# Kernel tuning notes

Measured on AMD Instinct MI355X. Metric: run time of the kernel, lower is better.

The kernel has to match this reference:

```python
import jax, jax.numpy as jnp
import numpy as np

D = 1024
H = 4
HD = D // H
B = 256
L = 64
DILATIONS = (1, 4, 8, 16)


def setup_inputs() -> dict:
    key = jax.random.key(0)
    ks = jax.random.split(key, 12)
    s = 1.0 / np.sqrt(D)
    return {
        "x": jax.random.normal(ks[0], (B, D), jnp.float32),
        "hist": jax.random.normal(ks[1], (L, B, D), jnp.float32),
        "Wq": jax.random.normal(ks[2], (D, D), jnp.float32) * s,
        "bq": jnp.zeros((D,), jnp.float32),
        "Wk": jax.random.normal(ks[3], (D, D), jnp.float32) * s,
        "bk": jnp.zeros((D,), jnp.float32),
        "Wv": jax.random.normal(ks[4], (D, D), jnp.float32) * s,
        "bv": jnp.zeros((D,), jnp.float32),
        "Wo": jax.random.normal(ks[5], (D, D), jnp.float32) * s,
        "bo": jnp.zeros((D,), jnp.float32),
        "dil_w": jnp.full((len(DILATIONS),), 1.0 / len(DILATIONS), jnp.float32),
        "gamma": jnp.ones((D,), jnp.float32),
        "beta": jnp.zeros((D,), jnp.float32),
    }


def reference(x, hist, Wq, bq, Wk, bk, Wv, bv, Wo, bo, dil_w, gamma, beta):
    scale = 1.0 / np.sqrt(HD)
    q = (x @ Wq + bq).reshape(B, H, HD)  # (B, H, HD)
    attended = []
    for d in DILATIONS:
        # history frames at stride d, concatenated along dim 0 (faithful to torch.cat)
        frames = hist[::d].reshape(-1, D)              # (T', D), T' = ceil(L/d)*B
        k = (frames @ Wk + bk).reshape(-1, H, HD)      # (T', H, HD)
        v = (frames @ Wv + bv).reshape(-1, H, HD)
        s = jnp.einsum('bhd,thd->bht', q, k) * scale   # (B, H, T')
        a = jax.nn.softmax(s, axis=-1)
        attended.append(jnp.einsum('bht,thd->bhd', a, v).reshape(B, D))
    w = jax.nn.softmax(dil_w, axis=0)
    combined = sum(w[i] * attended[i] for i in range(len(DILATIONS)))
    y = x + combined @ Wo + bo
    mu = jnp.mean(y, axis=-1, keepdims=True)
    var = jnp.var(y, axis=-1, keepdims=True)
    return (y - mu) / jnp.sqrt(var + 1e-5) * gamma + beta
```

## Files before the change

kernel.cpp:

```cpp
#include <hip/hip_runtime.h>


#define DD    1024
#define TALL  16384

typedef _Float16 half8  __attribute__((ext_vector_type(8)));
typedef _Float16 half4v __attribute__((ext_vector_type(4)));
typedef float    floatx4 __attribute__((ext_vector_type(4)));
typedef unsigned int u32;

static const size_t OFF_WQT = 0;
static const size_t OFF_WKT = 2097152;
static const size_t OFF_WVT = 4194304;
static const size_t OFF_WOT = 6291456;
static const size_t OFF_XB  = 8388608;
static const size_t OFF_QS  = 8912896;
static const size_t OFF_HB  = 16777216;
static const size_t OFF_S   = OFF_HB;
static const size_t OFF_KB  = 50331648;
static const size_t OFF_VT  = 83886080;
static const size_t OFF_PART= 117440512;
static const size_t OFF_MT  = 134217728;
static const size_t OFF_CT  = 134221824;
static const size_t OFF_CB  = 134483968;
static const size_t OFF_CP  = 135008256;

__device__ __forceinline__ void gl_lds16(const void* g, void* l) {
  __builtin_amdgcn_global_load_lds((const __attribute__((address_space(1))) u32*)g,
                                   (__attribute__((address_space(3))) u32*)l, 16, 0, 0);
}

__global__ void wtrans_kernel(const float* __restrict__ W0, const float* __restrict__ W1,
                              const float* __restrict__ W2, const float* __restrict__ W3,
                              _Float16* __restrict__ T0, _Float16* __restrict__ T1,
                              _Float16* __restrict__ T2, _Float16* __restrict__ T3) {
  const float* W; _Float16* T;
  switch (blockIdx.z) {
    case 0: W = W0; T = T0; break;
    case 1: W = W1; T = T1; break;
    case 2: W = W2; T = T2; break;
    default: W = W3; T = T3; break;
  }
  __shared__ float tile[32][33];
  int tx = threadIdx.x & 31, ty = threadIdx.x >> 5;
  int k0 = blockIdx.x * 32, n0 = blockIdx.y * 32;
#pragma unroll
  for (int i = 0; i < 4; i++) {
    int r = ty + i * 8;
    tile[r][tx] = W[(size_t)(k0 + r) * DD + n0 + tx];
  }
  __syncthreads();
#pragma unroll
  for (int i = 0; i < 4; i++) {
    int r = ty + i * 8;
    T[(size_t)(n0 + r) * DD + k0 + tx] = (_Float16)tile[tx][r];
  }
}

__global__ void cvt_kernel(const float* __restrict__ in, _Float16* __restrict__ out, int n4) {
  int i = blockIdx.x * 256 + threadIdx.x;
  if (i >= n4) return;
  float4 v = ((const float4*)in)[i];
  half4v h = {(_Float16)v.x, (_Float16)v.y, (_Float16)v.z, (_Float16)v.w};
  *(half4v*)(out + 4 * (size_t)i) = h;
}

__device__ __forceinline__ void gemm_core(const _Float16* __restrict__ A, size_t lda,
                                          const _Float16* __restrict__ B, size_t ldb,
                                          int kIters, _Float16* As, _Float16* Bs,
                                          int tid, floatx4 acc[4][4]) {
  int lane = tid & 63, w = tid >> 6;
  int l15 = lane & 15, quad = lane >> 4;
  int wm = (w >> 1) * 64, wn = (w & 1) * 64;
  const char* gA0 = (const char*)(A + (size_t)(tid >> 2) * lda + (tid & 3) * 8);
  const char* gA1 = (const char*)(A + ((size_t)(tid >> 2) + 64) * lda + (tid & 3) * 8);
  const char* gB0 = (const char*)(B + (size_t)(tid >> 2) * ldb + (tid & 3) * 8);
  const char* gB1 = (const char*)(B + ((size_t)(tid >> 2) + 64) * ldb + (tid & 3) * 8);
  _Float16* lA0 = As + w * 512; _Float16* lA1 = As + 2048 + w * 512;
  _Float16* lB0 = Bs + w * 512; _Float16* lB1 = Bs + 2048 + w * 512;
  for (int kk = 0; kk < kIters; kk++) {
    __syncthreads();
    size_t off = (size_t)kk * 64;
    gl_lds16(gA0 + off, lA0);
    gl_lds16(gA1 + off, lA1);
    gl_lds16(gB0 + off, lB0);
    gl_lds16(gB1 + off, lB1);
    __syncthreads();
    half8 a[4];
#pragma unroll
    for (int mi = 0; mi < 4; mi++) a[mi] = *(const half8*)&As[(wm + mi * 16 + l15) * 32 + quad * 8];
#pragma unroll
    for (int ni = 0; ni < 4; ni++) {
      half8 b8 = *(const half8*)&Bs[(wn + ni * 16 + l15) * 32 + quad * 8];
#pragma unroll
      for (int mi = 0; mi < 4; mi++)
        acc[mi][ni] = __builtin_amdgcn_mfma_f32_16x16x32_f16(a[mi], b8, acc[mi][ni], 0, 0, 0);
    }
  }
}

template <bool OUTF32>
__launch_bounds__(256, 2)
__global__ void gemm_f16_kernel(const _Float16* __restrict__ A, size_t lda, size_t aoffz,
                                const _Float16* __restrict__ B, size_t ldb, size_t boffz,
                                int kIters, const float* __restrict__ bias, float scale,
                                void* __restrict__ C, size_t ldc, size_t coffz) {
  __shared__ __align__(16) _Float16 As[4096];
  __shared__ __align__(16) _Float16 Bs[4096];
  int tid = threadIdx.x;
  const _Float16* Ab = A + aoffz * blockIdx.z + (size_t)(blockIdx.y * 128) * lda;
  const _Float16* Bb = B + boffz * blockIdx.z + (size_t)(blockIdx.x * 128) * ldb;
  floatx4 acc[4][4];
  floatx4 zero = {0.f, 0.f, 0.f, 0.f};
#pragma unroll
  for (int a = 0; a < 4; a++)
#pragma unroll
    for (int b = 0; b < 4; b++) acc[a][b] = zero;
  gemm_core(Ab, lda, Bb, ldb, kIters, As, Bs, tid, acc);
  int lane = tid & 63, w = tid >> 6;
  int l15 = lane & 15, quad = lane >> 4;
  int wm = (w >> 1) * 64, wn = (w & 1) * 64;
#pragma unroll
  for (int mi = 0; mi < 4; mi++)
#pragma unroll
    for (int ni = 0; ni < 4; ni++) {
      int colg = blockIdx.x * 128 + wn + ni * 16 + l15;
      float bv = bias ? bias[colg] : 0.f;
#pragma unroll
      for (int r = 0; r < 4; r++) {
        int rowg = blockIdx.y * 128 + wm + mi * 16 + quad * 4 + r;
        float v = (acc[mi][ni][r] + bv) * scale;
        size_t idx = coffz * blockIdx.z + (size_t)rowg * ldc + colg;
        if (OUTF32) ((float*)C)[idx] = v;
        else ((_Float16*)C)[idx] = (_Float16)v;
      }
    }
}

__launch_bounds__(256, 2)
__global__ void gemm_kv_kernel(const _Float16* __restrict__ A,
                               const _Float16* __restrict__ WkT, const _Float16* __restrict__ WvT,
                               const float* __restrict__ bk, const float* __restrict__ bv,
                               _Float16* __restrict__ K, _Float16* __restrict__ Vt) {
  __shared__ __align__(16) _Float16 As[4096];
  __shared__ __align__(16) _Float16 Bk[4096];
  __shared__ __align__(16) _Float16 Bv[4096];
  int tid = threadIdx.x;
  int lane = tid & 63, w = tid >> 6;
  int l15 = lane & 15, quad = lane >> 4;
  int wm = (w >> 1) * 64, wn = (w & 1) * 64;
  int m0 = blockIdx.y * 128, n0 = blockIdx.x * 128;
  floatx4 accK[4][4], accV[4][4];
  floatx4 zero = {0.f, 0.f, 0.f, 0.f};
#pragma unroll
  for (int a = 0; a < 4; a++)
#pragma unroll
    for (int b = 0; b < 4; b++) { accK[a][b] = zero; accV[a][b] = zero; }
  const char* gA0 = (const char*)(A + ((size_t)m0 + (tid >> 2)) * 1024 + (tid & 3) * 8);
  const char* gA1 = gA0 + 64 * 1024 * 2;
  const char* gK0 = (const char*)(WkT + ((size_t)n0 + (tid >> 2)) * 1024 + (tid & 3) * 8);
  const char* gK1 = gK0 + 64 * 1024 * 2;
  const char* gV0 = (const char*)(WvT + ((size_t)n0 + (tid >> 2)) * 1024 + (tid & 3) * 8);
  const char* gV1 = gV0 + 64 * 1024 * 2;
  _Float16* lA0 = As + w * 512; _Float16* lA1 = As + 2048 + w * 512;
  _Float16* lK0 = Bk + w * 512; _Float16* lK1 = Bk + 2048 + w * 512;
  _Float16* lV0 = Bv + w * 512; _Float16* lV1 = Bv + 2048 + w * 512;
  for (int kk = 0; kk < 32; kk++) {
    __syncthreads();
    size_t off = (size_t)kk * 64;
    gl_lds16(gA0 + off, lA0); gl_lds16(gA1 + off, lA1);
    gl_lds16(gK0 + off, lK0); gl_lds16(gK1 + off, lK1);
    gl_lds16(gV0 + off, lV0); gl_lds16(gV1 + off, lV1);
    __syncthreads();
    half8 a[4];
#pragma unroll
    for (int mi = 0; mi < 4; mi++) a[mi] = *(const half8*)&As[(wm + mi * 16 + l15) * 32 + quad * 8];
#pragma unroll
    for (int ni = 0; ni < 4; ni++) {
      half8 k8 = *(const half8*)&Bk[(wn + ni * 16 + l15) * 32 + quad * 8];
      half8 v8 = *(const half8*)&Bv[(wn + ni * 16 + l15) * 32 + quad * 8];
#pragma unroll
      for (int mi = 0; mi < 4; mi++) {
        accK[mi][ni] = __builtin_amdgcn_mfma_f32_16x16x32_f16(a[mi], k8, accK[mi][ni], 0, 0, 0);
        accV[mi][ni] = __builtin_amdgcn_mfma_f32_16x16x32_f16(a[mi], v8, accV[mi][ni], 0, 0, 0);
      }
    }
  }
#pragma unroll
  for (int mi = 0; mi < 4; mi++)
#pragma unroll
    for (int ni = 0; ni < 4; ni++) {
      int col = n0 + wn + ni * 16 + l15;
      float bkv = bk[col], bvv = bv[col];
#pragma unroll
      for (int r = 0; r < 4; r++) {
        int row = m0 + wm + mi * 16 + quad * 4 + r;
        K[(size_t)row * 1024 + col] = (_Float16)(accK[mi][ni][r] + bkv);
        Vt[(size_t)col * TALL + row] = (_Float16)(accV[mi][ni][r] + bvv);
      }
    }
}

__global__ void stats_kernel(const _Float16* __restrict__ S, const float* __restrict__ dil_w,
                             float* __restrict__ m_tab, float* __restrict__ c_tab) {
  int r = blockIdx.x;
  const _Float16* row = S + (size_t)r * TALL;
  int tid = threadIdx.x;
  half8 v[8];
  float mloc = -1e30f;
#pragma unroll
  for (int i = 0; i < 8; i++) {
    v[i] = *(const half8*)&row[tid * 64 + i * 8];
#pragma unroll
    for (int j = 0; j < 8; j++) mloc = fmaxf(mloc, (float)v[i][j]);
  }
  __shared__ float sred[256];
  __shared__ float Z[4];
  sred[tid] = mloc;
  __syncthreads();
  for (int sft = 128; sft >= 1; sft >>= 1) {
    if (tid < sft) sred[tid] = fmaxf(sred[tid], sred[tid + sft]);
    __syncthreads();
  }
  float m = sred[0];
  if (tid < 4) Z[tid] = 0.f;
  __syncthreads();
  float es = 0.f;
#pragma unroll
  for (int i = 0; i < 8; i++)
#pragma unroll
    for (int j = 0; j < 8; j++) es += __expf((float)v[i][j] - m);
  float fs = es;
  fs += __shfl_xor(fs, 1, 64);
  fs += __shfl_xor(fs, 2, 64);
  int f = tid >> 2;
  if ((tid & 3) == 0) {
    atomicAdd(&Z[0], fs);
    if ((f & 3) == 0) atomicAdd(&Z[1], fs);
    if ((f & 7) == 0) atomicAdd(&Z[2], fs);
    if ((f & 15) == 0) atomicAdd(&Z[3], fs);
  }
  __syncthreads();
  if (tid < 64) {
    float w0 = dil_w[0], w1 = dil_w[1], w2 = dil_w[2], w3 = dil_w[3];
    float wmx = fmaxf(fmaxf(w0, w1), fmaxf(w2, w3));
    float e0 = __expf(w0 - wmx), e1 = __expf(w1 - wmx), e2 = __expf(w2 - wmx), e3 = __expf(w3 - wmx);
    float wsum = e0 + e1 + e2 + e3;
    float c = (e0 / wsum) / Z[0];
    if ((tid & 3) == 0) c += (e1 / wsum) / Z[1];
    if ((tid & 7) == 0) c += (e2 / wsum) / Z[2];
    if ((tid & 15) == 0) c += (e3 / wsum) / Z[3];
    c_tab[r * 64 + tid] = c * 256.0f;
  }
  if (tid == 0) m_tab[r] = m;
}

__global__ void pwrite_kernel(_Float16* __restrict__ S, const float* __restrict__ m_tab,
                              const float* __restrict__ c_tab) {
  size_t e = ((size_t)blockIdx.x * 256 + threadIdx.x) * 8;
  int r = (int)(e >> 14);
  int f = (int)((e & 16383) >> 8);
  float m = m_tab[r];
  float c = c_tab[r * 64 + f];
  half8 v = *(half8*)&S[e];
  half8 o;
#pragma unroll
  for (int j = 0; j < 8; j++) o[j] = (_Float16)(__expf((float)v[j] - m) * c);
  *(half8*)&S[e] = o;
}

__launch_bounds__(256, 2)
__global__ void gemm_pv_kernel(const _Float16* __restrict__ P, const _Float16* __restrict__ Vt,
                               float* __restrict__ part) {
  __shared__ __align__(16) _Float16 As[4096];
  __shared__ __align__(16) _Float16 Bs[4096];
  int tid = threadIdx.x;
  int h = blockIdx.z >> 4, sp = blockIdx.z & 15;
  const _Float16* Ab = P + (size_t)h * 4194304 + (size_t)(blockIdx.y * 128) * TALL + sp * 1024;
  const _Float16* Bb = Vt + (size_t)(h * 256 + blockIdx.x * 128) * TALL + sp * 1024;
  floatx4 acc[4][4];
  floatx4 zero = {0.f, 0.f, 0.f, 0.f};
#pragma unroll
  for (int a = 0; a < 4; a++)
#pragma unroll
    for (int b = 0; b < 4; b++) acc[a][b] = zero;
  gemm_core(Ab, TALL, Bb, TALL, 32, As, Bs, tid, acc);
  int lane = tid & 63, w = tid >> 6;
  int l15 = lane & 15, quad = lane >> 4;
  int wm = (w >> 1) * 64, wn = (w & 1) * 64;
#pragma unroll
  for (int mi = 0; mi < 4; mi++)
#pragma unroll
    for (int ni = 0; ni < 4; ni++) {
      int featg = h * 256 + blockIdx.x * 128 + wn + ni * 16 + l15;
#pragma unroll
      for (int r = 0; r < 4; r++) {
        int q = blockIdx.y * 128 + wm + mi * 16 + quad * 4 + r;
        part[((size_t)(sp * 256 + q)) * 1024 + featg] = acc[mi][ni][r];
      }
    }
}

__global__ void reduce_kernel(const float* __restrict__ part, _Float16* __restrict__ comb) {
  int q = blockIdx.x;
  int f4 = threadIdx.x * 4;
  float4 s = {0.f, 0.f, 0.f, 0.f};
  for (int sp = 0; sp < 16; sp++) {
    float4 p = *(const float4*)&part[((size_t)(sp * 256 + q)) * 1024 + f4];
    s.x += p.x; s.y += p.y; s.z += p.z; s.w += p.w;
  }
  const float inv = 1.f / 256.f;
  half4v o = {(_Float16)(s.x * inv), (_Float16)(s.y * inv), (_Float16)(s.z * inv), (_Float16)(s.w * inv)};
  *(half4v*)&comb[(size_t)q * 1024 + f4] = o;
}

__global__ void ln_kernel(const float* __restrict__ x, const float* __restrict__ cproj,
                          const float* __restrict__ gamma, const float* __restrict__ beta,
                          float* __restrict__ out) {
  int b = blockIdx.x, t = threadIdx.x;
  __shared__ float red[8];
  float y[4];
  float sum = 0.f, sq = 0.f;
#pragma unroll
  for (int i = 0; i < 4; i++) {
    int j = t + i * 256;
    y[i] = x[(size_t)b * 1024 + j] + cproj[(size_t)b * 1024 + j];
    sum += y[i];
    sq += y[i] * y[i];
  }
#pragma unroll
  for (int off = 1; off < 64; off <<= 1) {
    sum += __shfl_xor(sum, off, 64);
    sq += __shfl_xor(sq, off, 64);
  }
  int w = t >> 6, lane = t & 63;
  if (lane == 0) { red[w] = sum; red[4 + w] = sq; }
  __syncthreads();
  sum = red[0] + red[1] + red[2] + red[3];
  sq = red[4] + red[5] + red[6] + red[7];
  float mu = sum * (1.f / 1024.f);
  float var = sq * (1.f / 1024.f) - mu * mu;
  float inv = rsqrtf(var + 1e-5f);
#pragma unroll
  for (int i = 0; i < 4; i++) {
    int j = t + i * 256;
    out[(size_t)b * 1024 + j] = (y[i] - mu) * inv * gamma[j] + beta[j];
  }
}

extern "C" void kernel_launch(void* const* d_in, const int* in_sizes, int n_in,
                              void* d_out, int out_size, void* d_ws, size_t ws_size,
                              hipStream_t stream) {
  const float* x     = (const float*)d_in[0];
  const float* hist  = (const float*)d_in[1];
  const float* Wq    = (const float*)d_in[2];
  const float* bq    = (const float*)d_in[3];
  const float* Wk    = (const float*)d_in[4];
  const float* bk    = (const float*)d_in[5];
  const float* Wv    = (const float*)d_in[6];
  const float* bv    = (const float*)d_in[7];
  const float* Wo    = (const float*)d_in[8];
  const float* bo    = (const float*)d_in[9];
  const float* dil_w = (const float*)d_in[10];
  const float* gamma = (const float*)d_in[11];
  const float* beta  = (const float*)d_in[12];
  char* ws = (char*)d_ws;

  _Float16* WqT   = (_Float16*)(ws + OFF_WQT);
  _Float16* WkT   = (_Float16*)(ws + OFF_WKT);
  _Float16* WvT   = (_Float16*)(ws + OFF_WVT);
  _Float16* WoT   = (_Float16*)(ws + OFF_WOT);
  _Float16* xb    = (_Float16*)(ws + OFF_XB);
  _Float16* Qs    = (_Float16*)(ws + OFF_QS);
  _Float16* histb = (_Float16*)(ws + OFF_HB);
  _Float16* Sb    = (_Float16*)(ws + OFF_S);
  _Float16* Kb    = (_Float16*)(ws + OFF_KB);
  _Float16* Vtb   = (_Float16*)(ws + OFF_VT);
  float* part     = (float*)(ws + OFF_PART);
  float* m_tab    = (float*)(ws + OFF_MT);
  float* c_tab    = (float*)(ws + OFF_CT);
  _Float16* comb  = (_Float16*)(ws + OFF_CB);
  float* cproj    = (float*)(ws + OFF_CP);

  wtrans_kernel<<<dim3(32, 32, 4), 256, 0, stream>>>(Wq, Wk, Wv, Wo, WqT, WkT, WvT, WoT);
  cvt_kernel<<<dim3(16384), 256, 0, stream>>>(hist, histb, 16777216 / 4);
  cvt_kernel<<<dim3(256), 256, 0, stream>>>(x, xb, 262144 / 4);
  gemm_f16_kernel<false><<<dim3(8, 2, 1), 256, 0, stream>>>(
      xb, 1024, 0, WqT, 1024, 0, 32, bq, 0.0625f, (void*)Qs, 1024, 0);
  gemm_kv_kernel<<<dim3(8, 128), 256, 0, stream>>>(histb, WkT, WvT, bk, bv, Kb, Vtb);
  gemm_f16_kernel<false><<<dim3(128, 2, 4), 256, 0, stream>>>(
      Qs, 1024, 256, Kb, 1024, 256, 8, nullptr, 1.0f, (void*)Sb, TALL, 4194304);
  stats_kernel<<<dim3(1024), 256, 0, stream>>>(Sb, dil_w, m_tab, c_tab);
  pwrite_kernel<<<dim3(8192), 256, 0, stream>>>(Sb, m_tab, c_tab);
  gemm_pv_kernel<<<dim3(2, 2, 64), 256, 0, stream>>>(Sb, Vtb, part);
  reduce_kernel<<<dim3(256), 256, 0, stream>>>(part, comb);
  gemm_f16_kernel<true><<<dim3(8, 2, 1), 256, 0, stream>>>(
      comb, 1024, 0, WoT, 1024, 0, 32, bo, 1.0f, (void*)cproj, 1024, 0);
  ln_kernel<<<dim3(256), 256, 0, stream>>>(x, cproj, gamma, beta, (float*)d_out);
}
```

Measured before the change: 338.4 us.

## Fuse softmax stats and write, swizzle LDS, split-K PV and output GEMMs

Merges the softmax statistics and probability-write kernels into one kernel that keeps the row in registers, so the score matrix is read once instead of twice. An XOR swizzle is applied to the LDS tile layout in the GEMMs to reduce bank conflicts. The PV GEMM split-K factor is doubled for more parallelism, and the output projection is split-K by four, with its partial sums and bias folded into the layernorm kernel. Also merges the two convert kernels, vectorizes the V-transpose stores, and raises launch bounds to three blocks per CU.

```diff
diff --git a/kernel.cpp b/kernel.cpp
--- a/kernel.cpp
+++ b/kernel.cpp
@@ -18,12 +18,10 @@
 static const size_t OFF_HB  = 16777216;
 static const size_t OFF_S   = OFF_HB;
 static const size_t OFF_KB  = 50331648;
+static const size_t OFF_PVP = OFF_KB;
 static const size_t OFF_VT  = 83886080;
-static const size_t OFF_PART= 117440512;
-static const size_t OFF_MT  = 134217728;
-static const size_t OFF_CT  = 134221824;
+static const size_t OFF_OPP = 117440512;
 static const size_t OFF_CB  = 134483968;
-static const size_t OFF_CP  = 135008256;
 
 __device__ __forceinline__ void gl_lds16(const void* g, void* l) {
   __builtin_amdgcn_global_load_lds((const __attribute__((address_space(1))) u32*)g,
@@ -57,12 +55,15 @@
   }
 }
 
-__global__ void cvt_kernel(const float* __restrict__ in, _Float16* __restrict__ out, int n4) {
+__global__ void cvt2_kernel(const float* __restrict__ a, _Float16* __restrict__ oa, int na4,
+                            const float* __restrict__ b, _Float16* __restrict__ ob, int nb4) {
   int i = blockIdx.x * 256 + threadIdx.x;
-  if (i >= n4) return;
-  float4 v = ((const float4*)in)[i];
+  const float* src; _Float16* dst;
+  if (i < na4) { src = a; dst = oa; }
+  else { i -= na4; if (i >= nb4) return; src = b; dst = ob; }
+  float4 v = ((const float4*)src)[i];
   half4v h = {(_Float16)v.x, (_Float16)v.y, (_Float16)v.z, (_Float16)v.w};
-  *(half4v*)(out + 4 * (size_t)i) = h;
+  *(half4v*)(dst + 4 * (size_t)i) = h;
 }
 
 __device__ __forceinline__ void gemm_core(const _Float16* __restrict__ A, size_t lda,
@@ -72,10 +73,12 @@
   int lane = tid & 63, w = tid >> 6;
   int l15 = lane & 15, quad = lane >> 4;
   int wm = (w >> 1) * 64, wn = (w & 1) * 64;
-  const char* gA0 = (const char*)(A + (size_t)(tid >> 2) * lda + (tid & 3) * 8);
-  const char* gA1 = (const char*)(A + ((size_t)(tid >> 2) + 64) * lda + (tid & 3) * 8);
-  const char* gB0 = (const char*)(B + (size_t)(tid >> 2) * ldb + (tid & 3) * 8);
-  const char* gB1 = (const char*)(B + ((size_t)(tid >> 2) + 64) * ldb + (tid & 3) * 8);
+  int swz = ((tid & 3) ^ ((tid >> 3) & 3)) * 8;
+  int pch = (quad ^ ((l15 >> 1) & 3)) * 8;
+  const char* gA0 = (const char*)(A + (size_t)(tid >> 2) * lda + swz);
+  const char* gA1 = (const char*)(A + ((size_t)(tid >> 2) + 64) * lda + swz);
+  const char* gB0 = (const char*)(B + (size_t)(tid >> 2) * ldb + swz);
+  const char* gB1 = (const char*)(B + ((size_t)(tid >> 2) + 64) * ldb + swz);
   _Float16* lA0 = As + w * 512; _Float16* lA1 = As + 2048 + w * 512;
   _Float16* lB0 = Bs + w * 512; _Float16* lB1 = Bs + 2048 + w * 512;
   for (int kk = 0; kk < kIters; kk++) {
@@ -88,10 +91,10 @@
     __syncthreads();
     half8 a[4];
 #pragma unroll
-    for (int mi = 0; mi < 4; mi++) a[mi] = *(const half8*)&As[(wm + mi * 16 + l15) * 32 + quad * 8];
+    for (int mi = 0; mi < 4; mi++) a[mi] = *(const half8*)&As[(wm + mi * 16 + l15) * 32 + pch];
 #pragma unroll
     for (int ni = 0; ni < 4; ni++) {
-      half8 b8 = *(const half8*)&Bs[(wn + ni * 16 + l15) * 32 + quad * 8];
+      half8 b8 = *(const half8*)&Bs[(wn + ni * 16 + l15) * 32 + pch];
 #pragma unroll
       for (int mi = 0; mi < 4; mi++)
         acc[mi][ni] = __builtin_amdgcn_mfma_f32_16x16x32_f16(a[mi], b8, acc[mi][ni], 0, 0, 0);
@@ -100,7 +103,7 @@
 }
 
 template <bool OUTF32>
-__launch_bounds__(256, 2)
+__launch_bounds__(256, 3)
 __global__ void gemm_f16_kernel(const _Float16* __restrict__ A, size_t lda, size_t aoffz,
                                 const _Float16* __restrict__ B, size_t ldb, size_t boffz,
                                 int kIters, const float* __restrict__ bias, float scale,
@@ -150,17 +153,19 @@
   int l15 = lane & 15, quad = lane >> 4;
   int wm = (w >> 1) * 64, wn = (w & 1) * 64;
   int m0 = blockIdx.y * 128, n0 = blockIdx.x * 128;
+  int swz = ((tid & 3) ^ ((tid >> 3) & 3)) * 8;
+  int pch = (quad ^ ((l15 >> 1) & 3)) * 8;
   floatx4 accK[4][4], accV[4][4];
   floatx4 zero = {0.f, 0.f, 0.f, 0.f};
 #pragma unroll
   for (int a = 0; a < 4; a++)
 #pragma unroll
     for (int b = 0; b < 4; b++) { accK[a][b] = zero; accV[a][b] = zero; }
-  const char* gA0 = (const char*)(A + ((size_t)m0 + (tid >> 2)) * 1024 + (tid & 3) * 8);
+  const char* gA0 = (const char*)(A + ((size_t)m0 + (tid >> 2)) * 1024 + swz);
   const char* gA1 = gA0 + 64 * 1024 * 2;
-  const char* gK0 = (const char*)(WkT + ((size_t)n0 + (tid >> 2)) * 1024 + (tid & 3) * 8);
+  const char* gK0 = (const char*)(WkT + ((size_t)n0 + (tid >> 2)) * 1024 + swz);
   const char* gK1 = gK0 + 64 * 1024 * 2;
-  const char* gV0 = (const char*)(WvT + ((size_t)n0 + (tid >> 2)) * 1024 + (tid & 3) * 8);
+  const char* gV0 = (const char*)(WvT + ((size_t)n0 + (tid >> 2)) * 1024 + swz);
   const char* gV1 = gV0 + 64 * 1024 * 2;
   _Float16* lA0 = As + w * 512; _Float16* lA1 = As + 2048 + w * 512;
   _Float16* lK0 = Bk + w * 512; _Float16* lK1 = Bk + 2048 + w * 512;
@@ -174,11 +179,11 @@
     __syncthreads();
     half8 a[4];
 #pragma unroll
-    for (int mi = 0; mi < 4; mi++) a[mi] = *(const half8*)&As[(wm + mi * 16 + l15) * 32 + quad * 8];
+    for (int mi = 0; mi < 4; mi++) a[mi] = *(const half8*)&As[(wm + mi * 16 + l15) * 32 + pch];
 #pragma unroll
     for (int ni = 0; ni < 4; ni++) {
-      half8 k8 = *(const half8*)&Bk[(wn + ni * 16 + l15) * 32 + quad * 8];
-      half8 v8 = *(const half8*)&Bv[(wn + ni * 16 + l15) * 32 + quad * 8];
+      half8 k8 = *(const half8*)&Bk[(wn + ni * 16 + l15) * 32 + pch];
+      half8 v8 = *(const half8*)&Bv[(wn + ni * 16 + l15) * 32 + pch];
 #pragma unroll
       for (int mi = 0; mi < 4; mi++) {
         accK[mi][ni] = __builtin_amdgcn_mfma_f32_16x16x32_f16(a[mi], k8, accK[mi][ni], 0, 0, 0);
@@ -192,53 +197,58 @@
     for (int ni = 0; ni < 4; ni++) {
       int col = n0 + wn + ni * 16 + l15;
       float bkv = bk[col], bvv = bv[col];
-#pragma unroll
-      for (int r = 0; r < 4; r++) {
-        int row = m0 + wm + mi * 16 + quad * 4 + r;
-        K[(size_t)row * 1024 + col] = (_Float16)(accK[mi][ni][r] + bkv);
-        Vt[(size_t)col * TALL + row] = (_Float16)(accV[mi][ni][r] + bvv);
-      }
+      int row0 = m0 + wm + mi * 16 + quad * 4;
+#pragma unroll
+      for (int r = 0; r < 4; r++)
+        K[(size_t)(row0 + r) * 1024 + col] = (_Float16)(accK[mi][ni][r] + bkv);
+      half4v vv = {(_Float16)(accV[mi][ni][0] + bvv), (_Float16)(accV[mi][ni][1] + bvv),
+                   (_Float16)(accV[mi][ni][2] + bvv), (_Float16)(accV[mi][ni][3] + bvv)};
+      *(half4v*)&Vt[(size_t)col * TALL + row0] = vv;
     }
 }
 
-__global__ void stats_kernel(const _Float16* __restrict__ S, const float* __restrict__ dil_w,
-                             float* __restrict__ m_tab, float* __restrict__ c_tab) {
-  int r = blockIdx.x;
-  const _Float16* row = S + (size_t)r * TALL;
-  int tid = threadIdx.x;
+__global__ void softmax_kernel(_Float16* __restrict__ S, const float* __restrict__ dil_w) {
+  int r = blockIdx.x, tid = threadIdx.x;
+  _Float16* row = S + (size_t)r * TALL;
+  int lane = tid & 63, w = tid >> 6;
   half8 v[8];
   float mloc = -1e30f;
 #pragma unroll
   for (int i = 0; i < 8; i++) {
-    v[i] = *(const half8*)&row[tid * 64 + i * 8];
+    v[i] = *(const half8*)&row[((size_t)i * 256 + tid) * 8];
 #pragma unroll
     for (int j = 0; j < 8; j++) mloc = fmaxf(mloc, (float)v[i][j]);
   }
-  __shared__ float sred[256];
-  __shared__ float Z[4];
-  sred[tid] = mloc;
-  __syncthreads();
-  for (int sft = 128; sft >= 1; sft >>= 1) {
-    if (tid < sft) sred[tid] = fmaxf(sred[tid], sred[tid + sft]);
-    __syncthreads();
-  }
-  float m = sred[0];
-  if (tid < 4) Z[tid] = 0.f;
-  __syncthreads();
-  float es = 0.f;
-#pragma unroll
-  for (int i = 0; i < 8; i++)
-#pragma unroll
-    for (int j = 0; j < 8; j++) es += __expf((float)v[i][j] - m);
-  float fs = es;
-  fs += __shfl_xor(fs, 1, 64);
-  fs += __shfl_xor(fs, 2, 64);
-  int f = tid >> 2;
-  if ((tid & 3) == 0) {
-    atomicAdd(&Z[0], fs);
-    if ((f & 3) == 0) atomicAdd(&Z[1], fs);
-    if ((f & 7) == 0) atomicAdd(&Z[2], fs);
-    if ((f & 15) == 0) atomicAdd(&Z[3], fs);
+  __shared__ float wmax[4];
+  __shared__ float Zf[64];
+  __shared__ float Zd[4];
+  __shared__ float cf[64];
+#pragma unroll
+  for (int off = 1; off <= 32; off <<= 1) mloc = fmaxf(mloc, __shfl_xor(mloc, off, 64));
+  if (lane == 0) wmax[w] = mloc;
+  __syncthreads();
+  float m = fmaxf(fmaxf(wmax[0], wmax[1]), fmaxf(wmax[2], wmax[3]));
+  float es[8];
+#pragma unroll
+  for (int i = 0; i < 8; i++) {
+    float s = 0.f;
+#pragma unroll
+    for (int j = 0; j < 8; j++) s += __expf((float)v[i][j] - m);
+#pragma unroll
+    for (int off = 1; off <= 16; off <<= 1) s += __shfl_xor(s, off, 64);
+    es[i] = s;
+  }
+  if ((lane & 31) == 0) {
+    int half = tid >> 5;
+#pragma unroll
+    for (int i = 0; i < 8; i++) Zf[i * 8 + half] = es[i];
+  }
+  __syncthreads();
+  if (tid < 4) {
+    int step = 1 << (tid + (tid ? 1 : 0));
+    float z = 0.f;
+    for (int f = 0; f < 64; f += step) z += Zf[f];
+    Zd[tid] = z;
   }
   __syncthreads();
   if (tid < 64) {
@@ -246,45 +256,39 @@
     float wmx = fmaxf(fmaxf(w0, w1), fmaxf(w2, w3));
     float e0 = __expf(w0 - wmx), e1 = __expf(w1 - wmx), e2 = __expf(w2 - wmx), e3 = __expf(w3 - wmx);
     float wsum = e0 + e1 + e2 + e3;
-    float c = (e0 / wsum) / Z[0];
-    if ((tid & 3) == 0) c += (e1 / wsum) / Z[1];
-    if ((tid & 7) == 0) c += (e2 / wsum) / Z[2];
-    if ((tid & 15) == 0) c += (e3 / wsum) / Z[3];
-    c_tab[r * 64 + tid] = c * 256.0f;
-  }
-  if (tid == 0) m_tab[r] = m;
-}
-
-__global__ void pwrite_kernel(_Float16* __restrict__ S, const float* __restrict__ m_tab,
-                              const float* __restrict__ c_tab) {
-  size_t e = ((size_t)blockIdx.x * 256 + threadIdx.x) * 8;
-  int r = (int)(e >> 14);
-  int f = (int)((e & 16383) >> 8);
-  float m = m_tab[r];
-  float c = c_tab[r * 64 + f];
-  half8 v = *(half8*)&S[e];
-  half8 o;
-#pragma unroll
-  for (int j = 0; j < 8; j++) o[j] = (_Float16)(__expf((float)v[j] - m) * c);
-  *(half8*)&S[e] = o;
-}
-
-__launch_bounds__(256, 2)
+    float c = (e0 / wsum) / Zd[0];
+    if ((tid & 3) == 0) c += (e1 / wsum) / Zd[1];
+    if ((tid & 7) == 0) c += (e2 / wsum) / Zd[2];
+    if ((tid & 15) == 0) c += (e3 / wsum) / Zd[3];
+    cf[tid] = c * 256.0f;
+  }
+  __syncthreads();
+#pragma unroll
+  for (int i = 0; i < 8; i++) {
+    float c = cf[i * 8 + (tid >> 5)];
+    half8 o;
+#pragma unroll
+    for (int j = 0; j < 8; j++) o[j] = (_Float16)(__expf((float)v[i][j] - m) * c);
+    *(half8*)&row[((size_t)i * 256 + tid) * 8] = o;
+  }
+}
+
+__launch_bounds__(256, 3)
 __global__ void gemm_pv_kernel(const _Float16* __restrict__ P, const _Float16* __restrict__ Vt,
                                float* __restrict__ part) {
   __shared__ __align__(16) _Float16 As[4096];
   __shared__ __align__(16) _Float16 Bs[4096];
   int tid = threadIdx.x;
-  int h = blockIdx.z >> 4, sp = blockIdx.z & 15;
-  const _Float16* Ab = P + (size_t)h * 4194304 + (size_t)(blockIdx.y * 128) * TALL + sp * 1024;
-  const _Float16* Bb = Vt + (size_t)(h * 256 + blockIdx.x * 128) * TALL + sp * 1024;
+  int h = blockIdx.z >> 5, sp = blockIdx.z & 31;
+  const _Float16* Ab = P + (size_t)h * 4194304 + (size_t)(blockIdx.y * 128) * TALL + sp * 512;
+  const _Float16* Bb = Vt + (size_t)(h * 256 + blockIdx.x * 128) * TALL + sp * 512;
   floatx4 acc[4][4];
   floatx4 zero = {0.f, 0.f, 0.f, 0.f};
 #pragma unroll
   for (int a = 0; a < 4; a++)
 #pragma unroll
     for (int b = 0; b < 4; b++) acc[a][b] = zero;
-  gemm_core(Ab, TALL, Bb, TALL, 32, As, Bs, tid, acc);
+  gemm_core(Ab, TALL, Bb, TALL, 16, As, Bs, tid, acc);
   int lane = tid & 63, w = tid >> 6;
   int l15 = lane & 15, quad = lane >> 4;
   int wm = (w >> 1) * 64, wn = (w & 1) * 64;
@@ -305,7 +309,7 @@
   int q = blockIdx.x;
   int f4 = threadIdx.x * 4;
   float4 s = {0.f, 0.f, 0.f, 0.f};
-  for (int sp = 0; sp < 16; sp++) {
+  for (int sp = 0; sp < 32; sp++) {
     float4 p = *(const float4*)&part[((size_t)(sp * 256 + q)) * 1024 + f4];
     s.x += p.x; s.y += p.y; s.z += p.z; s.w += p.w;
   }
@@ -314,9 +318,9 @@
   *(half4v*)&comb[(size_t)q * 1024 + f4] = o;
 }
 
-__global__ void ln_kernel(const float* __restrict__ x, const float* __restrict__ cproj,
-                          const float* __restrict__ gamma, const float* __restrict__ beta,
-                          float* __restrict__ out) {
+__global__ void ln_kernel(const float* __restrict__ x, const float* __restrict__ part2,
+                          const float* __restrict__ bo, const float* __restrict__ gamma,
+                          const float* __restrict__ beta, float* __restrict__ out) {
   int b = blockIdx.x, t = threadIdx.x;
   __shared__ float red[8];
   float y[4];
@@ -324,9 +328,12 @@
 #pragma unroll
   for (int i = 0; i < 4; i++) {
     int j = t + i * 256;
-    y[i] = x[(size_t)b * 1024 + j] + cproj[(size_t)b * 1024 + j];
-    sum += y[i];
-    sq += y[i] * y[i];
+    float v = x[(size_t)b * 1024 + j] + bo[j];
+#pragma unroll
+    for (int z = 0; z < 4; z++) v += part2[(size_t)z * 262144 + (size_t)b * 1024 + j];
+    y[i] = v;
+    sum += v;
+    sq += v * v;
   }
 #pragma unroll
   for (int off = 1; off < 64; off <<= 1) {
@@ -376,25 +383,21 @@
   _Float16* Sb    = (_Float16*)(ws + OFF_S);
   _Float16* Kb    = (_Float16*)(ws + OFF_KB);
   _Float16* Vtb   = (_Float16*)(ws + OFF_VT);
-  float* part     = (float*)(ws + OFF_PART);
-  float* m_tab    = (float*)(ws + OFF_MT);
-  float* c_tab    = (float*)(ws + OFF_CT);
+  float* pvpart   = (float*)(ws + OFF_PVP);
+  float* oppart   = (float*)(ws + OFF_OPP);
   _Float16* comb  = (_Float16*)(ws + OFF_CB);
-  float* cproj    = (float*)(ws + OFF_CP);
 
   wtrans_kernel<<<dim3(32, 32, 4), 256, 0, stream>>>(Wq, Wk, Wv, Wo, WqT, WkT, WvT, WoT);
-  cvt_kernel<<<dim3(16384), 256, 0, stream>>>(hist, histb, 16777216 / 4);
-  cvt_kernel<<<dim3(256), 256, 0, stream>>>(x, xb, 262144 / 4);
+  cvt2_kernel<<<dim3(16640), 256, 0, stream>>>(hist, histb, 4194304, x, xb, 65536);
   gemm_f16_kernel<false><<<dim3(8, 2, 1), 256, 0, stream>>>(
       xb, 1024, 0, WqT, 1024, 0, 32, bq, 0.0625f, (void*)Qs, 1024, 0);
   gemm_kv_kernel<<<dim3(8, 128), 256, 0, stream>>>(histb, WkT, WvT, bk, bv, Kb, Vtb);
   gemm_f16_kernel<false><<<dim3(128, 2, 4), 256, 0, stream>>>(
       Qs, 1024, 256, Kb, 1024, 256, 8, nullptr, 1.0f, (void*)Sb, TALL, 4194304);
-  stats_kernel<<<dim3(1024), 256, 0, stream>>>(Sb, dil_w, m_tab, c_tab);
-  pwrite_kernel<<<dim3(8192), 256, 0, stream>>>(Sb, m_tab, c_tab);
-  gemm_pv_kernel<<<dim3(2, 2, 64), 256, 0, stream>>>(Sb, Vtb, part);
-  reduce_kernel<<<dim3(256), 256, 0, stream>>>(part, comb);
-  gemm_f16_kernel<true><<<dim3(8, 2, 1), 256, 0, stream>>>(
-      comb, 1024, 0, WoT, 1024, 0, 32, bo, 1.0f, (void*)cproj, 1024, 0);
-  ln_kernel<<<dim3(256), 256, 0, stream>>>(x, cproj, gamma, beta, (float*)d_out);
-}
+  softmax_kernel<<<dim3(1024), 256, 0, stream>>>(Sb, dil_w);
+  gemm_pv_kernel<<<dim3(2, 2, 128), 256, 0, stream>>>(Sb, Vtb, pvpart);
+  reduce_kernel<<<dim3(256), 256, 0, stream>>>(pvpart, comb);
+  gemm_f16_kernel<true><<<dim3(8, 2, 4), 256, 0, stream>>>(
+      comb, 1024, 256, WoT, 1024, 256, 8, nullptr, 1.0f, (void*)oppart, 1024, 262144);
+  ln_kernel<<<dim3(256), 256, 0, stream>>>(x, oppart, bo, gamma, beta, (float*)d_out);
+}
```

Measured after the change: 327.4 us. 3.2% less time.
